# Kernel optimization log

Hardware: AMD Instinct MI355X
Metric: run time of the kernel (lower is better)

## Reference

```python
import jax, jax.numpy as jnp
import numpy as np

D_MODEL = 1024
N_HEAD = 16
D_HEAD = D_MODEL // N_HEAD
FFN_HIDDEN = 4096
NEG_INF = -1e30


def sinusoid_pos_emb(pos_seq, d_model):
    # pos_seq: [K] descending relative positions; returns [K, d_model]
    inv_freq = 1.0 / (10000.0 ** (jnp.arange(0, d_model, 2, dtype=jnp.float32) / d_model))
    ang = pos_seq[:, None] * inv_freq[None, :]
    return jnp.concatenate([jnp.sin(ang), jnp.cos(ang)], axis=-1)


def rel_shift(x):
    # x: [B, H, Q, K] -> Transformer-XL relative shift
    b, h, q, k = x.shape
    x = jnp.pad(x, ((0, 0), (0, 0), (0, 0), (1, 0)))
    x = x.reshape(b, h, k + 1, q)[:, :, 1:, :].reshape(b, h, q, k)
    return x


def layer_norm(x, g, b, eps=1e-5):
    mu = jnp.mean(x, axis=-1, keepdims=True)
    var = jnp.var(x, axis=-1, keepdims=True)
    return (x - mu) * jax.lax.rsqrt(var + eps) * g + b


def setup_inputs() -> dict:
    key = jax.random.key(0)
    ks = jax.random.split(key, 20)
    B, T, M = 4, 2048, 2048
    s = 0.02
    inp = {
        "x": jax.random.normal(ks[0], (B, T, D_MODEL), jnp.float32),
        "mem": jax.random.normal(ks[1], (B, M, D_MODEL), jnp.float32),
        "Wq": jax.random.normal(ks[2], (D_MODEL, D_MODEL), jnp.float32) * s,
        "bq": jnp.zeros((D_MODEL,), jnp.float32),
        "Wk": jax.random.normal(ks[3], (D_MODEL, D_MODEL), jnp.float32) * s,
        "bk": jnp.zeros((D_MODEL,), jnp.float32),
        "Wv": jax.random.normal(ks[4], (D_MODEL, D_MODEL), jnp.float32) * s,
        "bv": jnp.zeros((D_MODEL,), jnp.float32),
        "Wo": jax.random.normal(ks[5], (D_MODEL, D_MODEL), jnp.float32) * s,
        "bo": jnp.zeros((D_MODEL,), jnp.float32),
        "Wr": jax.random.normal(ks[6], (D_MODEL, D_MODEL), jnp.float32) * s,
        "u": jax.random.normal(ks[7], (N_HEAD, D_HEAD), jnp.float32) * s,
        "v": jax.random.normal(ks[8], (N_HEAD, D_HEAD), jnp.float32) * s,
        "g1": jnp.ones((D_MODEL,), jnp.float32),
        "be1": jnp.zeros((D_MODEL,), jnp.float32),
        "g2": jnp.ones((D_MODEL,), jnp.float32),
        "be2": jnp.zeros((D_MODEL,), jnp.float32),
        "W1": jax.random.normal(ks[9], (D_MODEL, FFN_HIDDEN), jnp.float32) * s,
        "b1": jnp.zeros((FFN_HIDDEN,), jnp.float32),
        "W2": jax.random.normal(ks[10], (FFN_HIDDEN, D_MODEL), jnp.float32) * s,
        "b2": jnp.zeros((D_MODEL,), jnp.float32),
        "is_causal": 1,
    }
    return inp


def xl_attention(x, mem, Wq, bq, Wk, bk, Wv, bv, Wo, bo, Wr, u, v, is_causal):
    B, T, D = x.shape
    M = mem.shape[1]
    K = M + T
    c = jnp.concatenate([mem, x], axis=1)  # [B, K, D]
    q = (x @ Wq + bq).reshape(B, T, N_HEAD, D_HEAD)
    k = (c @ Wk + bk).reshape(B, K, N_HEAD, D_HEAD)
    vv = (c @ Wv + bv).reshape(B, K, N_HEAD, D_HEAD)
    pos_seq = jnp.arange(K - 1, -1, -1, dtype=jnp.float32)
    r = (sinusoid_pos_emb(pos_seq, D) @ Wr).reshape(K, N_HEAD, D_HEAD)
    # content term + relative-position term (Transformer-XL eq. A+C and B+D)
    AC = jnp.einsum('bihd,bjhd->bhij', q + u, k)
    BD = rel_shift(jnp.einsum('bihd,jhd->bhij', q + v, r))
    score = (AC + BD) * (1.0 / np.sqrt(D_HEAD))
    if is_causal:
        i = jnp.arange(T)[:, None]
        j = jnp.arange(K)[None, :]
        causal = (j <= i + M)  # query i may attend keys up to its own position
        score = jnp.where(causal[None, None], score, NEG_INF)
    attn = jax.nn.softmax(score, axis=-1)
    out = jnp.einsum('bhij,bjhd->bihd', attn, vv).reshape(B, T, D)
    return out @ Wo + bo


def reference(x, mem, Wq, bq, Wk, bk, Wv, bv, Wo, bo, Wr, u, v,
              g1, be1, g2, be2, W1, b1, W2, b2, is_causal):
    # dropout is identity at inference
    a = xl_attention(x, mem, Wq, bq, Wk, bk, Wv, bv, Wo, bo, Wr, u, v, is_causal)
    h = layer_norm(a + x, g1, be1)
    f = jax.nn.gelu(h @ W1 + b1) @ W2 + b2
    return layer_norm(f + h, g2, be2)
```

## Files before the change

kernel.cpp:

```cpp
#include <hip/hip_runtime.h>
#include <stdint.h>

typedef unsigned short u16;
typedef short s16x8 __attribute__((ext_vector_type(8)));
typedef unsigned short u16x4 __attribute__((ext_vector_type(4)));
typedef float f32x4 __attribute__((ext_vector_type(4)));

#define DEV static __device__ __forceinline__

DEV u16 f2b(float f) {
  union { float f; unsigned u; } v; v.f = f;
  unsigned r = v.u + 0x7fffu + ((v.u >> 16) & 1u);
  return (u16)(r >> 16);
}
DEV float b2f(u16 b) {
  union { unsigned u; float f; } v; v.u = ((unsigned)b) << 16; return v.f;
}
DEV unsigned pk_trunc(float a, float b) {
  return __builtin_amdgcn_perm(__float_as_uint(b), __float_as_uint(a), 0x07060302u);
}
DEV f32x4 MFMA16(s16x8 a, s16x8 b, f32x4 c) {
  return __builtin_amdgcn_mfma_f32_16x16x32_bf16(a, b, c, 0, 0, 0);
}
#define GLD_LDS16(gp, lp)                                                            \
  __builtin_amdgcn_global_load_lds((const __attribute__((address_space(1))) void*)(gp), \
                                   (__attribute__((address_space(3))) void*)(lp), 16, 0, 0)


__global__ __launch_bounds__(256) void wt_cast_t(const float* __restrict__ W,
                                                 u16* __restrict__ Wt, int Kd, int Nd) {
  __shared__ float tile[32][33];
  const int n0 = blockIdx.x * 32, k0 = blockIdx.y * 32;
  const int t = threadIdx.x;
#pragma unroll
  for (int p = 0; p < 4; ++p) {
    int idx = p * 256 + t; int r = idx >> 5, c = idx & 31;
    tile[r][c] = W[(long)(k0 + r) * Nd + n0 + c];
  }
  __syncthreads();
#pragma unroll
  for (int p = 0; p < 4; ++p) {
    int idx = p * 256 + t; int r = idx >> 5, c = idx & 31;
    Wt[(long)(n0 + r) * Kd + k0 + c] = f2b(tile[c][r]);
  }
}

__global__ __launch_bounds__(256) void build_cb(const float* __restrict__ x,
                                                const float* __restrict__ mem,
                                                u16* __restrict__ cb) {
  long idx = (long)blockIdx.x * 256 + threadIdx.x;
  long e4 = idx * 4;
  int b = (int)(e4 >> 22);
  long rem = e4 & ((1L << 22) - 1);
  int tok = (int)(rem >> 10);
  int d = (int)(rem & 1023);
  const float* src = (tok < 2048) ? &mem[((long)b * 2048 + tok) * 1024 + d]
                                  : &x[((long)b * 2048 + (tok - 2048)) * 1024 + d];
  float4 vv = *(const float4*)src;
  uint2 o;
  o.x = (unsigned)f2b(vv.x) | ((unsigned)f2b(vv.y) << 16);
  o.y = (unsigned)f2b(vv.z) | ((unsigned)f2b(vv.w) << 16);
  *(uint2*)&cb[e4] = o;
}

__global__ __launch_bounds__(256) void pos_emb(u16* __restrict__ pe) {
  const int d = blockIdx.x;
  const int e0 = threadIdx.x * 4;
  u16 o[4];
#pragma unroll
  for (int i = 0; i < 4; ++i) {
    int e = e0 + i;
    int f = (e < 512) ? e : (e - 512);
    float invf = expf(-(float)f * (9.210340371976184f / 512.f));
    float ang = (float)d * invf;
    o[i] = f2b((e < 512) ? sinf(ang) : cosf(ang));
  }
  uint2 pk; pk.x = (unsigned)o[0] | ((unsigned)o[1] << 16);
  pk.y = (unsigned)o[2] | ((unsigned)o[3] << 16);
  *(uint2*)&pe[(long)d * 1024 + e0] = pk;
}

#define EPI_BF16 0
#define EPI_F32 1
#define EPI_GELU 2
#define EPI_VT 3

template <int EPI, int QMAP>
__global__ __launch_bounds__(256) void gemm_bt(const u16* __restrict__ A,
                                               const u16* __restrict__ Bt,
                                               const float* __restrict__ bias,
                                               void* __restrict__ outp, int Ndim, int Kdim) {
  __shared__ __align__(16) u16 As[128 * 32];
  __shared__ __align__(16) u16 Bs[128 * 32];
  const int col0 = blockIdx.x * 128;
  const int row0 = blockIdx.y * 128;
  const int t = threadIdx.x;
  const int w = t >> 6, l = t & 63;
  const int wr = (w >> 1) * 64, wc = (w & 1) * 64;
  const int lr = l & 15, lk = (l >> 4) * 8;
  f32x4 acc[4][4];
#pragma unroll
  for (int m = 0; m < 4; ++m)
#pragma unroll
    for (int n = 0; n < 4; ++n) acc[m][n] = f32x4{0.f, 0.f, 0.f, 0.f};

  for (int k0 = 0; k0 < Kdim; k0 += 32) {
#pragma unroll
    for (int it = 0; it < 2; ++it) {
      int c = it * 256 + t;
      int r = c >> 2, e = (c & 3) * 8;
      long ga = row0 + r;
      if (QMAP) ga = ((ga >> 11) << 12) + 2048 + (ga & 2047);
      GLD_LDS16(A + ga * Kdim + k0 + e, &As[c * 8]);
      GLD_LDS16(Bt + (long)(col0 + r) * Kdim + k0 + e, &Bs[c * 8]);
    }
    __syncthreads();
    s16x8 af[4], bfv[4];
#pragma unroll
    for (int m = 0; m < 4; ++m) af[m] = *(const s16x8*)&As[(wr + m * 16 + lr) * 32 + lk];
#pragma unroll
    for (int n = 0; n < 4; ++n) bfv[n] = *(const s16x8*)&Bs[(wc + n * 16 + lr) * 32 + lk];
#pragma unroll
    for (int m = 0; m < 4; ++m)
#pragma unroll
      for (int n = 0; n < 4; ++n) acc[m][n] = MFMA16(af[m], bfv[n], acc[m][n]);
    __syncthreads();
  }

  const int lg = (l >> 4) * 4;
#pragma unroll
  for (int m = 0; m < 4; ++m) {
    int rbase = row0 + wr + m * 16 + lg;
#pragma unroll
    for (int n = 0; n < 4; ++n) {
      int gc = col0 + wc + n * 16 + lr;
      float bv = bias ? bias[gc] : 0.f;
#pragma unroll
      for (int rg = 0; rg < 4; ++rg) {
        int grow = rbase + rg;
        float vv = acc[m][n][rg] + bv;
        if (EPI == EPI_GELU) {
          float x3 = vv * vv * vv;
          vv = 0.5f * vv * (1.f + tanhf(0.7978845608028654f * (vv + 0.044715f * x3)));
        }
        if (EPI == EPI_F32) {
          ((float*)outp)[(long)grow * Ndim + gc] = vv;
        } else if (EPI == EPI_VT) {
          int bb = grow >> 12, tok = grow & 4095;
          int hh = gc >> 6, dd = gc & 63;
          ((u16*)outp)[((long)((bb * 16 + hh) * 64 + dd) << 12) + tok] = f2b(vv);
        } else {
          ((u16*)outp)[(long)grow * Ndim + gc] = f2b(vv);
        }
      }
    }
  }
}

#define SCALE_LOG2 0.18033688011111793f

__global__ __launch_bounds__(512, 4) void attn_fused(
    const u16* __restrict__ qg, const u16* __restrict__ kg, const u16* __restrict__ vTg,
    const u16* __restrict__ rg, const float* __restrict__ u, const float* __restrict__ vparam,
    const int* __restrict__ causal_p, u16* __restrict__ Og) {
  __shared__ __align__(16) u16 Ks[3][64 * 64];
  __shared__ __align__(16) u16 Vs[3][64 * 64];
  __shared__ __align__(16) u16 GPs[8][16 * 84];

  const int bh = blockIdx.x, b = bh >> 4, h = bh & 15;
  const int i0 = (int)(gridDim.y - 1 - blockIdx.y) * 128;
  const int t = threadIdx.x, w = t >> 6, l = t & 63;
  const int q = l & 15, g = l >> 4, lk = g * 8;
  const int causal = causal_p[0];

  const long kbase = ((long)b * 4096) * 1024 + h * 64;
  const long vbase = ((long)((b * 16 + h) * 64)) * 4096;

  const int irow = i0 + 16 * w + q;
  const u16* qp = qg + ((long)(b * 2048 + irow)) * 1024 + h * 64;
  s16x8 qlo = *(const s16x8*)(qp + lk);
  s16x8 qhi = *(const s16x8*)(qp + 32 + lk);
  s16x8 qu0, qu1, qv0, qv1;
#pragma unroll
  for (int j = 0; j < 8; ++j) {
    float a0 = b2f((u16)qlo[j]), a1 = b2f((u16)qhi[j]);
    float uu0 = u[h * 64 + lk + j], vv0 = vparam[h * 64 + lk + j];
    float uu1 = u[h * 64 + 32 + lk + j], vv1 = vparam[h * 64 + 32 + lk + j];
    qu0[j] = (short)f2b((a0 + uu0) * SCALE_LOG2); qv0[j] = (short)f2b((a0 + vv0) * SCALE_LOG2);
    qu1[j] = (short)f2b((a1 + uu1) * SCALE_LOG2); qv1[j] = (short)f2b((a1 + vv1) * SCALE_LOG2);
  }

  float lsum = 0.f;
  f32x4 oacc[4];
#pragma unroll
  for (int n = 0; n < 4; ++n) oacc[n] = f32x4{0.f, 0.f, 0.f, 0.f};

  u16* gpw = &GPs[w][0];
  const int kc0 = q * 64 + ((g ^ (q & 7)) << 3);
  const int kc1 = kc0 ^ 32;
  const int gq = q * 85 + 63;
  const int gst = q * 84 + 4 * g;
  const int pst = q * 72 + 4 * g;
  const int prd = q * 72 + lk;

  auto STAGE = [&](int j0s, int bufi) {
    int rrow = t >> 3, gch = (t & 7) ^ (rrow & 7);
    GLD_LDS16(kg + kbase + (long)(j0s + rrow) * 1024 + gch * 8, &Ks[bufi][t * 8]);
    GLD_LDS16(vTg + vbase + (long)rrow * 4096 + j0s + gch * 8, &Vs[bufi][t * 8]);
  };

  s16x8 rf0[5], rf1[5];
  auto LOADR = [&](int j0r) {
    const int dlo = 2048 + i0 + 16 * w - j0r - 63;
#pragma unroll
    for (int tt = 0; tt < 5; ++tt) {
      int d = dlo + tt * 16 + q; d = min(max(d, 0), 4095);
      const u16* rp = rg + ((long)d << 10) + h * 64;
      rf0[tt] = *(const s16x8*)(rp + lk);
      rf1[tt] = *(const s16x8*)(rp + 32 + lk);
    }
  };

  const int jmax = causal ? (2048 + i0 + 128) : 4096;
  const int nt = jmax >> 6;
  const int jlimit = 2048 + i0 + 16 * w + 15;
  STAGE(0, 0);
  if (nt > 1) STAGE(64, 1);
  LOADR(0);
  int cur = 0;

  for (int ti = 0; ti < nt; ++ti) {
    const int j0 = ti << 6;
    asm volatile("s_waitcnt vmcnt(12)" ::: "memory");
    __syncthreads();
    if (ti + 2 < nt) STAGE((ti + 2) << 6, cur == 0 ? 2 : cur - 1);

    if (!causal || j0 <= jlimit) {
      const u16* ksp = &Ks[cur][0];
      const u16* vsp = &Vs[cur][0];

      f32x4 sv[4];
      __builtin_amdgcn_s_setprio(1);
#pragma unroll
      for (int n = 0; n < 4; ++n) {
        s16x8 af0 = *(const s16x8*)&ksp[kc0 + n * 1024];
        s16x8 af1 = *(const s16x8*)&ksp[kc1 + n * 1024];
        f32x4 z = f32x4{0.f, 0.f, 0.f, 0.f};
        z = MFMA16(af0, qu0, z);
        z = MFMA16(af1, qu1, z);
        sv[n] = z;
      }
#pragma unroll
      for (int tt = 0; tt < 5; ++tt) {
        f32x4 z = f32x4{0.f, 0.f, 0.f, 0.f};
        z = MFMA16(rf0[tt], qv0, z);
        z = MFMA16(rf1[tt], qv1, z);
        uint2 gp2 = {pk_trunc(z[0], z[1]), pk_trunc(z[2], z[3])};
        *(u16x4*)&gpw[gst + tt * 16] = __builtin_bit_cast(u16x4, gp2);
      }
      __builtin_amdgcn_s_setprio(0);

      if (ti + 1 < nt && (!causal || j0 + 64 <= jlimit)) LOADR(j0 + 64);

      const bool need_mask = (causal != 0) && (j0 + 63 > 2048 + i0 + 16 * w);
#pragma unroll
      for (int n = 0; n < 4; ++n) {
#pragma unroll
        for (int r = 0; r < 4; ++r) {
          int j = 16 * n + 4 * g + r;
          float bd = b2f(gpw[gq - j]);
          float scv = sv[n][r] + bd;
          if (need_mask && (j0 + j > 2048 + irow)) scv = -3.0e38f;
          sv[n][r] = scv;
        }
      }
      float ls = 0.f;
#pragma unroll
      for (int n = 0; n < 4; ++n) {
        float p0 = __builtin_amdgcn_exp2f(sv[n][0]);
        float p1 = __builtin_amdgcn_exp2f(sv[n][1]);
        float p2 = __builtin_amdgcn_exp2f(sv[n][2]);
        float p3 = __builtin_amdgcn_exp2f(sv[n][3]);
        ls += (p0 + p1) + (p2 + p3);
        uint2 pp = {pk_trunc(p0, p1), pk_trunc(p2, p3)};
        *(u16x4*)&gpw[pst + n * 16] = __builtin_bit_cast(u16x4, pp);
      }
      lsum += ls;

      s16x8 pb0 = *(const s16x8*)&gpw[prd];
      s16x8 pb1 = *(const s16x8*)&gpw[prd + 32];
      __builtin_amdgcn_s_setprio(1);
#pragma unroll
      for (int n = 0; n < 4; ++n) {
        s16x8 va0 = *(const s16x8*)&vsp[kc0 + n * 1024];
        s16x8 va1 = *(const s16x8*)&vsp[kc1 + n * 1024];
        oacc[n] = MFMA16(va0, pb0, oacc[n]);
        oacc[n] = MFMA16(va1, pb1, oacc[n]);
      }
      __builtin_amdgcn_s_setprio(0);
    }
    cur = (cur == 2) ? 0 : cur + 1;
  }

  lsum += __shfl_xor(lsum, 16);
  lsum += __shfl_xor(lsum, 32);
  const float linv = 1.f / lsum;
  const long obase = (long)(b * 2048 + irow) * 1024 + h * 64;
#pragma unroll
  for (int n = 0; n < 4; ++n) {
    u16x4 ov = {f2b(oacc[n][0] * linv), f2b(oacc[n][1] * linv),
                f2b(oacc[n][2] * linv), f2b(oacc[n][3] * linv)};
    *(u16x4*)&Og[obase + n * 16 + 4 * g] = ov;
  }
}

template <int WRITE_BF16>
__global__ __launch_bounds__(256) void ln_res(const float* __restrict__ a,
                                              const float* __restrict__ resid,
                                              const float* __restrict__ g,
                                              const float* __restrict__ be,
                                              float* __restrict__ outf, u16* __restrict__ outb) {
  const int row = blockIdx.x;
  const int t = threadIdx.x;
  const long base = (long)row * 1024;
  float4 av = *(const float4*)&a[base + t * 4];
  float4 rv = *(const float4*)&resid[base + t * 4];
  float x0 = av.x + rv.x, x1 = av.y + rv.y, x2 = av.z + rv.z, x3 = av.w + rv.w;
  float s = x0 + x1 + x2 + x3;
  float q = x0 * x0 + x1 * x1 + x2 * x2 + x3 * x3;
#pragma unroll
  for (int d = 1; d < 64; d <<= 1) {
    s += __shfl_xor(s, d);
    q += __shfl_xor(q, d);
  }
  __shared__ float ss[4], sq[4];
  if ((t & 63) == 0) { ss[t >> 6] = s; sq[t >> 6] = q; }
  __syncthreads();
  s = ss[0] + ss[1] + ss[2] + ss[3];
  q = sq[0] + sq[1] + sq[2] + sq[3];
  float mu = s * (1.f / 1024.f);
  float var = q * (1.f / 1024.f) - mu * mu;
  float rstd = rsqrtf(var + 1e-5f);
  float4 gv = *(const float4*)&g[t * 4];
  float4 bv = *(const float4*)&be[t * 4];
  float y0 = (x0 - mu) * rstd * gv.x + bv.x;
  float y1 = (x1 - mu) * rstd * gv.y + bv.y;
  float y2 = (x2 - mu) * rstd * gv.z + bv.z;
  float y3 = (x3 - mu) * rstd * gv.w + bv.w;
  float4 ov = {y0, y1, y2, y3};
  *(float4*)&outf[base + t * 4] = ov;
  if (WRITE_BF16) {
    uint2 o;
    o.x = (unsigned)f2b(y0) | ((unsigned)f2b(y1) << 16);
    o.y = (unsigned)f2b(y2) | ((unsigned)f2b(y3) << 16);
    *(uint2*)&outb[base + t * 4] = o;
  }
}

extern "C" void kernel_launch(void* const* d_in, const int* in_sizes, int n_in, void* d_out,
                              int out_size, void* d_ws, size_t ws_size, hipStream_t stream) {
  const float* x = (const float*)d_in[0];
  const float* mem = (const float*)d_in[1];
  const float* Wq = (const float*)d_in[2];
  const float* bq = (const float*)d_in[3];
  const float* Wk = (const float*)d_in[4];
  const float* bk = (const float*)d_in[5];
  const float* Wv = (const float*)d_in[6];
  const float* bv = (const float*)d_in[7];
  const float* Wo = (const float*)d_in[8];
  const float* bo = (const float*)d_in[9];
  const float* Wr = (const float*)d_in[10];
  const float* u = (const float*)d_in[11];
  const float* vp = (const float*)d_in[12];
  const float* g1 = (const float*)d_in[13];
  const float* be1 = (const float*)d_in[14];
  const float* g2 = (const float*)d_in[15];
  const float* be2 = (const float*)d_in[16];
  const float* W1 = (const float*)d_in[17];
  const float* b1 = (const float*)d_in[18];
  const float* W2 = (const float*)d_in[19];
  const float* b2 = (const float*)d_in[20];
  const int* iscaus = (const int*)d_in[21];

  char* ws = (char*)d_ws;
  const size_t MB = 1024 * 1024;
  u16* WqT = (u16*)(ws + 0 * MB);
  u16* WkT = (u16*)(ws + 2 * MB);
  u16* WvT = (u16*)(ws + 4 * MB);
  u16* WoT = (u16*)(ws + 6 * MB);
  u16* WrT = (u16*)(ws + 8 * MB);
  u16* W1T = (u16*)(ws + 10 * MB);
  u16* W2T = (u16*)(ws + 18 * MB);
  u16* cb = (u16*)(ws + 26 * MB);
  float* proj = (float*)(ws + 26 * MB);
  u16* pe = (u16*)(ws + 58 * MB);
  u16* qb = (u16*)(ws + 66 * MB);
  u16* kb = (u16*)(ws + 82 * MB);
  u16* vT = (u16*)(ws + 114 * MB);
  u16* rb = (u16*)(ws + 146 * MB);
  u16* aO = (u16*)(ws + 154 * MB);
  u16* hb = (u16*)(ws + 154 * MB);
  u16* f1 = (u16*)(ws + 58 * MB);
  float* f2 = (float*)(ws + 122 * MB);
  (void)ws_size; (void)in_sizes; (void)n_in; (void)out_size;

  wt_cast_t<<<dim3(32, 32), 256, 0, stream>>>(Wq, WqT, 1024, 1024);
  wt_cast_t<<<dim3(32, 32), 256, 0, stream>>>(Wk, WkT, 1024, 1024);
  wt_cast_t<<<dim3(32, 32), 256, 0, stream>>>(Wv, WvT, 1024, 1024);
  wt_cast_t<<<dim3(32, 32), 256, 0, stream>>>(Wo, WoT, 1024, 1024);
  wt_cast_t<<<dim3(32, 32), 256, 0, stream>>>(Wr, WrT, 1024, 1024);
  wt_cast_t<<<dim3(128, 32), 256, 0, stream>>>(W1, W1T, 1024, 4096);
  wt_cast_t<<<dim3(32, 128), 256, 0, stream>>>(W2, W2T, 4096, 1024);

  build_cb<<<16384, 256, 0, stream>>>(x, mem, cb);
  pos_emb<<<4096, 256, 0, stream>>>(pe);

  gemm_bt<EPI_BF16, 1><<<dim3(8, 64), 256, 0, stream>>>(cb, WqT, bq, qb, 1024, 1024);
  gemm_bt<EPI_BF16, 0><<<dim3(8, 128), 256, 0, stream>>>(cb, WkT, bk, kb, 1024, 1024);
  gemm_bt<EPI_VT, 0><<<dim3(8, 128), 256, 0, stream>>>(cb, WvT, bv, vT, 1024, 1024);
  gemm_bt<EPI_BF16, 0><<<dim3(8, 32), 256, 0, stream>>>(pe, WrT, nullptr, rb, 1024, 1024);

  attn_fused<<<dim3(64, 16), 512, 0, stream>>>(qb, kb, vT, rb, u, vp, iscaus, aO);

  gemm_bt<EPI_F32, 0><<<dim3(8, 64), 256, 0, stream>>>(aO, WoT, bo, proj, 1024, 1024);
  ln_res<1><<<8192, 256, 0, stream>>>(proj, x, g1, be1, proj, hb);

  gemm_bt<EPI_GELU, 0><<<dim3(32, 64), 256, 0, stream>>>(hb, W1T, b1, f1, 4096, 1024);
  gemm_bt<EPI_F32, 0><<<dim3(8, 64), 256, 0, stream>>>(f1, W2T, b2, f2, 1024, 4096);
  ln_res<0><<<8192, 256, 0, stream>>>(f2, proj, g2, be2, (float*)d_out, nullptr);
}
```

Measured before the change: 1.020 ms.

## Pipeline relative-position GEMM one tile ahead and switch K/V to double buffering

The positional-score MFMA for the next key tile is now computed during the current iteration into a separate LDS buffer, so the current tile's scores only need an LDS read of precomputed values. R fragments are loaded two tiles ahead instead of one. The K/V staging drops from triple to double buffering, and the P buffer is split from the G buffer. This is meant to hide the relative-position GEMM and global-load latency behind other work, at the cost of a shallower K/V prefetch and more registers held live.

```diff
diff --git a/kernel.cpp b/kernel.cpp
--- a/kernel.cpp
+++ b/kernel.cpp
@@ -163,9 +163,10 @@
     const u16* __restrict__ qg, const u16* __restrict__ kg, const u16* __restrict__ vTg,
     const u16* __restrict__ rg, const float* __restrict__ u, const float* __restrict__ vparam,
     const int* __restrict__ causal_p, u16* __restrict__ Og) {
-  __shared__ __align__(16) u16 Ks[3][64 * 64];
-  __shared__ __align__(16) u16 Vs[3][64 * 64];
-  __shared__ __align__(16) u16 GPs[8][16 * 84];
+  __shared__ __align__(16) u16 Ks[2][64 * 64];
+  __shared__ __align__(16) u16 Vs[2][64 * 64];
+  __shared__ __align__(16) u16 Gs[8][16 * 84];
+  __shared__ __align__(16) u16 Ps[8][16 * 72];
 
   const int bh = blockIdx.x, b = bh >> 4, h = bh & 15;
   const int i0 = (int)(gridDim.y - 1 - blockIdx.y) * 128;
@@ -195,7 +196,8 @@
 #pragma unroll
   for (int n = 0; n < 4; ++n) oacc[n] = f32x4{0.f, 0.f, 0.f, 0.f};
 
-  u16* gpw = &GPs[w][0];
+  u16* gw = &Gs[w][0];
+  u16* pw = &Ps[w][0];
   const int kc0 = q * 64 + ((g ^ (q & 7)) << 3);
   const int kc1 = kc0 ^ 32;
   const int gq = q * 85 + 63;
@@ -221,23 +223,47 @@
     }
   };
 
+  auto GPROD = [&]() {
+#pragma unroll
+    for (int tt = 0; tt < 5; ++tt) {
+      f32x4 z = f32x4{0.f, 0.f, 0.f, 0.f};
+      z = MFMA16(rf0[tt], qv0, z);
+      z = MFMA16(rf1[tt], qv1, z);
+      uint2 gp2 = {pk_trunc(z[0], z[1]), pk_trunc(z[2], z[3])};
+      *(u16x4*)&gw[gst + tt * 16] = __builtin_bit_cast(u16x4, gp2);
+    }
+  };
+
   const int jmax = causal ? (2048 + i0 + 128) : 4096;
   const int nt = jmax >> 6;
   const int jlimit = 2048 + i0 + 16 * w + 15;
+
   STAGE(0, 0);
+  asm volatile("" ::: "memory");
   if (nt > 1) STAGE(64, 1);
+  asm volatile("" ::: "memory");
   LOADR(0);
+  GPROD();
+  if (nt > 1) LOADR(64);
   int cur = 0;
 
   for (int ti = 0; ti < nt; ++ti) {
     const int j0 = ti << 6;
-    asm volatile("s_waitcnt vmcnt(12)" ::: "memory");
+    if (ti + 1 < nt) asm volatile("s_waitcnt vmcnt(10)" ::: "memory");
+    else             asm volatile("s_waitcnt vmcnt(0)" ::: "memory");
     __syncthreads();
-    if (ti + 2 < nt) STAGE((ti + 2) << 6, cur == 0 ? 2 : cur - 1);
+    if (ti + 1 < nt) STAGE((ti + 1) << 6, cur ^ 1);
+    asm volatile("" ::: "memory");
 
     if (!causal || j0 <= jlimit) {
       const u16* ksp = &Ks[cur][0];
       const u16* vsp = &Vs[cur][0];
+
+      float bd[4][4];
+#pragma unroll
+      for (int n = 0; n < 4; ++n)
+#pragma unroll
+        for (int r = 0; r < 4; ++r) bd[n][r] = b2f(gw[gq - (16 * n + 4 * g + r)]);
 
       f32x4 sv[4];
       __builtin_amdgcn_s_setprio(1);
@@ -250,45 +276,30 @@
         z = MFMA16(af1, qu1, z);
         sv[n] = z;
       }
-#pragma unroll
-      for (int tt = 0; tt < 5; ++tt) {
-        f32x4 z = f32x4{0.f, 0.f, 0.f, 0.f};
-        z = MFMA16(rf0[tt], qv0, z);
-        z = MFMA16(rf1[tt], qv1, z);
-        uint2 gp2 = {pk_trunc(z[0], z[1]), pk_trunc(z[2], z[3])};
-        *(u16x4*)&gpw[gst + tt * 16] = __builtin_bit_cast(u16x4, gp2);
-      }
+      if ((ti + 1 < nt) && (!causal || j0 + 64 <= jlimit)) GPROD();
       __builtin_amdgcn_s_setprio(0);
-
-      if (ti + 1 < nt && (!causal || j0 + 64 <= jlimit)) LOADR(j0 + 64);
+      if ((ti + 2 < nt) && (!causal || j0 + 128 <= jlimit)) LOADR(j0 + 128);
 
       const bool need_mask = (causal != 0) && (j0 + 63 > 2048 + i0 + 16 * w);
+      float ls = 0.f;
 #pragma unroll
       for (int n = 0; n < 4; ++n) {
+        float p[4];
 #pragma unroll
         for (int r = 0; r < 4; ++r) {
           int j = 16 * n + 4 * g + r;
-          float bd = b2f(gpw[gq - j]);
-          float scv = sv[n][r] + bd;
+          float scv = sv[n][r] + bd[n][r];
           if (need_mask && (j0 + j > 2048 + irow)) scv = -3.0e38f;
-          sv[n][r] = scv;
+          p[r] = __builtin_amdgcn_exp2f(scv);
         }
-      }
-      float ls = 0.f;
-#pragma unroll
-      for (int n = 0; n < 4; ++n) {
-        float p0 = __builtin_amdgcn_exp2f(sv[n][0]);
-        float p1 = __builtin_amdgcn_exp2f(sv[n][1]);
-        float p2 = __builtin_amdgcn_exp2f(sv[n][2]);
-        float p3 = __builtin_amdgcn_exp2f(sv[n][3]);
-        ls += (p0 + p1) + (p2 + p3);
-        uint2 pp = {pk_trunc(p0, p1), pk_trunc(p2, p3)};
-        *(u16x4*)&gpw[pst + n * 16] = __builtin_bit_cast(u16x4, pp);
+        ls += (p[0] + p[1]) + (p[2] + p[3]);
+        uint2 pp = {pk_trunc(p[0], p[1]), pk_trunc(p[2], p[3])};
+        *(u16x4*)&pw[pst + n * 16] = __builtin_bit_cast(u16x4, pp);
       }
       lsum += ls;
 
-      s16x8 pb0 = *(const s16x8*)&gpw[prd];
-      s16x8 pb1 = *(const s16x8*)&gpw[prd + 32];
+      s16x8 pb0 = *(const s16x8*)&pw[prd];
+      s16x8 pb1 = *(const s16x8*)&pw[prd + 32];
       __builtin_amdgcn_s_setprio(1);
 #pragma unroll
       for (int n = 0; n < 4; ++n) {
@@ -299,7 +310,7 @@
       }
       __builtin_amdgcn_s_setprio(0);
     }
-    cur = (cur == 2) ? 0 : cur + 1;
+    cur ^= 1;
   }
 
   lsum += __shfl_xor(lsum, 16);
```

New measurement: 1.734 ms. +70.0%, slower.

## Widen GEMM K-tile with swizzled LDS and double-buffer attention K/V

Applied to the files above, without the earlier changes.

The GEMM kernel now stages 64-wide K slices instead of 32 and XOR-swizzles the 16-byte chunks in LDS. This halves the barriers per K and is meant to avoid bank conflicts on the fragment reads. The attention kernel drops from triple- to double-buffered K/V staging, merges the wait and barrier into one asm block, and moves the relative-position prefetch to the end of each iteration. The smaller shared-memory footprint may raise occupancy, but the prefetch distance shrinks and R loads are now issued even on masked-out causal tiles.

```diff
diff --git a/kernel.cpp b/kernel.cpp
--- a/kernel.cpp
+++ b/kernel.cpp
@@ -90,44 +90,53 @@
                                                const u16* __restrict__ Bt,
                                                const float* __restrict__ bias,
                                                void* __restrict__ outp, int Ndim, int Kdim) {
-  __shared__ __align__(16) u16 As[128 * 32];
-  __shared__ __align__(16) u16 Bs[128 * 32];
+  __shared__ __align__(16) u16 As[128 * 64];
+  __shared__ __align__(16) u16 Bs[128 * 64];
   const int col0 = blockIdx.x * 128;
   const int row0 = blockIdx.y * 128;
   const int t = threadIdx.x;
   const int w = t >> 6, l = t & 63;
   const int wr = (w >> 1) * 64, wc = (w & 1) * 64;
-  const int lr = l & 15, lk = (l >> 4) * 8;
+  const int lr = l & 15, g = l >> 4;
   f32x4 acc[4][4];
 #pragma unroll
   for (int m = 0; m < 4; ++m)
 #pragma unroll
     for (int n = 0; n < 4; ++n) acc[m][n] = f32x4{0.f, 0.f, 0.f, 0.f};
 
-  for (int k0 = 0; k0 < Kdim; k0 += 32) {
-#pragma unroll
-    for (int it = 0; it < 2; ++it) {
+  for (int k0 = 0; k0 < Kdim; k0 += 64) {
+#pragma unroll
+    for (int it = 0; it < 4; ++it) {
       int c = it * 256 + t;
-      int r = c >> 2, e = (c & 3) * 8;
+      int r = c >> 3, ch = (c & 7) ^ (r & 7);
       long ga = row0 + r;
       if (QMAP) ga = ((ga >> 11) << 12) + 2048 + (ga & 2047);
-      GLD_LDS16(A + ga * Kdim + k0 + e, &As[c * 8]);
-      GLD_LDS16(Bt + (long)(col0 + r) * Kdim + k0 + e, &Bs[c * 8]);
+      GLD_LDS16(A + ga * Kdim + k0 + ch * 8, &As[c * 8]);
+      GLD_LDS16(Bt + (long)(col0 + r) * Kdim + k0 + ch * 8, &Bs[c * 8]);
     }
     __syncthreads();
-    s16x8 af[4], bfv[4];
-#pragma unroll
-    for (int m = 0; m < 4; ++m) af[m] = *(const s16x8*)&As[(wr + m * 16 + lr) * 32 + lk];
-#pragma unroll
-    for (int n = 0; n < 4; ++n) bfv[n] = *(const s16x8*)&Bs[(wc + n * 16 + lr) * 32 + lk];
-#pragma unroll
-    for (int m = 0; m < 4; ++m)
-#pragma unroll
-      for (int n = 0; n < 4; ++n) acc[m][n] = MFMA16(af[m], bfv[n], acc[m][n]);
+#pragma unroll
+    for (int kk = 0; kk < 2; ++kk) {
+      s16x8 af[4], bfv[4];
+#pragma unroll
+      for (int m = 0; m < 4; ++m) {
+        int rm = wr + m * 16 + lr;
+        af[m] = *(const s16x8*)&As[rm * 64 + (((g + 4 * kk) ^ (rm & 7)) << 3)];
+      }
+#pragma unroll
+      for (int n = 0; n < 4; ++n) {
+        int rn = wc + n * 16 + lr;
+        bfv[n] = *(const s16x8*)&Bs[rn * 64 + (((g + 4 * kk) ^ (rn & 7)) << 3)];
+      }
+#pragma unroll
+      for (int m = 0; m < 4; ++m)
+#pragma unroll
+        for (int n = 0; n < 4; ++n) acc[m][n] = MFMA16(af[m], bfv[n], acc[m][n]);
+    }
     __syncthreads();
   }
 
-  const int lg = (l >> 4) * 4;
+  const int lg = g * 4;
 #pragma unroll
   for (int m = 0; m < 4; ++m) {
     int rbase = row0 + wr + m * 16 + lg;
@@ -163,8 +172,8 @@
     const u16* __restrict__ qg, const u16* __restrict__ kg, const u16* __restrict__ vTg,
     const u16* __restrict__ rg, const float* __restrict__ u, const float* __restrict__ vparam,
     const int* __restrict__ causal_p, u16* __restrict__ Og) {
-  __shared__ __align__(16) u16 Ks[3][64 * 64];
-  __shared__ __align__(16) u16 Vs[3][64 * 64];
+  __shared__ __align__(16) u16 Ks[2][64 * 64];
+  __shared__ __align__(16) u16 Vs[2][64 * 64];
   __shared__ __align__(16) u16 GPs[8][16 * 84];
 
   const int bh = blockIdx.x, b = bh >> 4, h = bh & 15;
@@ -224,18 +233,18 @@
   const int jmax = causal ? (2048 + i0 + 128) : 4096;
   const int nt = jmax >> 6;
   const int jlimit = 2048 + i0 + 16 * w + 15;
+
   STAGE(0, 0);
-  if (nt > 1) STAGE(64, 1);
   LOADR(0);
   int cur = 0;
 
   for (int ti = 0; ti < nt; ++ti) {
     const int j0 = ti << 6;
-    asm volatile("s_waitcnt vmcnt(12)" ::: "memory");
-    __syncthreads();
-    if (ti + 2 < nt) STAGE((ti + 2) << 6, cur == 0 ? 2 : cur - 1);
-
-    if (!causal || j0 <= jlimit) {
+    asm volatile("s_waitcnt vmcnt(10)\n\ts_barrier" ::: "memory");
+    if (ti + 1 < nt) STAGE((ti + 1) << 6, cur ^ 1);
+
+    const bool live = !causal || j0 <= jlimit;
+    if (live) {
       const u16* ksp = &Ks[cur][0];
       const u16* vsp = &Vs[cur][0];
 
@@ -259,8 +268,6 @@
         *(u16x4*)&gpw[gst + tt * 16] = __builtin_bit_cast(u16x4, gp2);
       }
       __builtin_amdgcn_s_setprio(0);
-
-      if (ti + 1 < nt && (!causal || j0 + 64 <= jlimit)) LOADR(j0 + 64);
 
       const bool need_mask = (causal != 0) && (j0 + 63 > 2048 + i0 + 16 * w);
 #pragma unroll
@@ -299,7 +306,8 @@
       }
       __builtin_amdgcn_s_setprio(0);
     }
-    cur = (cur == 2) ? 0 : cur + 1;
+    if (ti + 1 < nt) LOADR(j0 + 64);
+    cur ^= 1;
   }
 
   lsum += __shfl_xor(lsum, 16);
```

After: 1.060 ms. 1.04x slower.
